# Kernel optimization log

Hardware: AMD Instinct MI355X
Metric: run time of the kernel (lower is better)

Reference implementation:

```python
import jax, jax.numpy as jnp
import numpy as np

N = 100000
E = 1600000
IN_C = 128
OUT_C = 64
NEG_SLOPE = 0.2


def setup_inputs() -> dict:
    key = jax.random.key(0)
    k1, k2, k3, k4 = jax.random.split(key, 4)
    x = jax.random.normal(k1, (N, IN_C), dtype=jnp.float32)
    edge_index = jax.random.randint(k2, (2, E), 0, N, dtype=jnp.int64)
    # Linear weight as in torch nn.Linear (bias=False): W @ x -> x @ W.T
    W = jax.random.normal(k3, (OUT_C, IN_C), dtype=jnp.float32) * (1.0 / np.sqrt(IN_C))
    # attention vector a over [Wx_i || Wx_j]
    a = jax.random.normal(k4, (2 * OUT_C,), dtype=jnp.float32) * (1.0 / np.sqrt(2 * OUT_C))
    return {"x": x, "edge_index": edge_index, "W": W, "a": a}


def reference(x, edge_index, W, a):
    src = edge_index[0]  # [E] source nodes j
    dst = edge_index[1]  # [E] target nodes i

    Wx = x @ W.T                                   # [N, OUT_C]
    # per-node attention scores, gathered per edge (same math as a . [Wx_i||Wx_j])
    s_i = Wx @ a[:OUT_C]                           # [N]
    s_j = Wx @ a[OUT_C:]                           # [N]
    e = jax.nn.leaky_relu(s_i[dst] + s_j[src], NEG_SLOPE)  # [E]

    # segment softmax over edges grouped by target node
    m = jax.ops.segment_max(e, dst, num_segments=N)        # [N]
    m = jnp.where(jnp.isneginf(m), 0.0, m)
    exp_e = jnp.exp(e - m[dst])                            # [E]
    denom = jax.ops.segment_sum(exp_e, dst, num_segments=N)  # [N]
    alpha = exp_e / denom[dst]                             # [E]

    msg = alpha[:, None] * Wx[src]                 # [E, OUT_C]
    h = jax.ops.segment_sum(msg, dst, num_segments=N)  # [N, OUT_C]
    return jax.nn.elu(h)
```

## Files before the change

### kernel.cpp

```cpp
#include <hip/hip_runtime.h>

#define NN 100000
#define EE 1600000
#define INC 128
#define OUTC 64
#define NEG_SLOPE 0.2f

#define BSH 7
#define BNODES 128
#define NB 782
#define BCAP 2560
#define SCAP2 4480
#define CHUNKA 4096
#define NBLKA 391
#define NBLKG (NB + NBLKA)
#define NSLOT 10

typedef __attribute__((ext_vector_type(8))) short bf16x8;
typedef __attribute__((ext_vector_type(4))) float f32x4;

__device__ __forceinline__ unsigned short f2bf(float f) {
  unsigned u = __float_as_uint(f);
  unsigned r = (u + 0x7fffu + ((u >> 16) & 1u)) >> 16;
  return (unsigned short)r;
}
__device__ __forceinline__ float bf2f(unsigned u16) {
  return __uint_as_float(u16 << 16);
}

__global__ __launch_bounds__(256) void k_zero(int* __restrict__ gcursor) {
  for (int i = threadIdx.x; i < NB; i += 256) gcursor[i] = 0;
}

__global__ __launch_bounds__(256)
__attribute__((amdgpu_waves_per_eu(1, 3)))
void k_gb(
    const float* __restrict__ x, const float* __restrict__ W,
    const float* __restrict__ a, unsigned short* __restrict__ Wxh,
    float* __restrict__ s_i, float* __restrict__ s_j,
    const int* __restrict__ src, const int* __restrict__ dst,
    int* __restrict__ gcursor, unsigned* __restrict__ binned)
{
  __shared__ __align__(16) char smem[44240];
  const int t = threadIdx.x;
  const int bid = blockIdx.x;
  const bool isBin = (bid % 3 == 2);

  if (!isBin) {
    const int gi = (bid / 3) * 2 + (bid % 3);
    unsigned short (*hs)[32][72] = reinterpret_cast<unsigned short(*)[32][72]>(smem);
    const int w = t >> 6;
    const int l = t & 63;
    const int lr = l & 15;
    const int lk = l >> 4;
    const int row0 = gi * 128 + w * 32;

    f32x4 acc[2][4];
    #pragma unroll
    for (int m = 0; m < 2; ++m)
      #pragma unroll
      for (int n = 0; n < 4; ++n) acc[m][n] = (f32x4){0.f, 0.f, 0.f, 0.f};

    #pragma unroll
    for (int ks = 0; ks < 4; ++ks) {
      const int k0 = ks * 32 + lk * 8;
      bf16x8 af[2], bfr[4];
      #pragma unroll
      for (int m = 0; m < 2; ++m) {
        int r = row0 + m * 16 + lr;
        r = (r < NN) ? r : (NN - 1);
        const float* p = &x[(size_t)r * INC + k0];
        float4 u0 = *reinterpret_cast<const float4*>(p);
        float4 u1 = *reinterpret_cast<const float4*>(p + 4);
        af[m][0] = (short)f2bf(u0.x); af[m][1] = (short)f2bf(u0.y);
        af[m][2] = (short)f2bf(u0.z); af[m][3] = (short)f2bf(u0.w);
        af[m][4] = (short)f2bf(u1.x); af[m][5] = (short)f2bf(u1.y);
        af[m][6] = (short)f2bf(u1.z); af[m][7] = (short)f2bf(u1.w);
      }
      #pragma unroll
      for (int n = 0; n < 4; ++n) {
        int c = n * 16 + lr;
        const float* p = &W[(size_t)c * INC + k0];
        float4 u0 = *reinterpret_cast<const float4*>(p);
        float4 u1 = *reinterpret_cast<const float4*>(p + 4);
        bfr[n][0] = (short)f2bf(u0.x); bfr[n][1] = (short)f2bf(u0.y);
        bfr[n][2] = (short)f2bf(u0.z); bfr[n][3] = (short)f2bf(u0.w);
        bfr[n][4] = (short)f2bf(u1.x); bfr[n][5] = (short)f2bf(u1.y);
        bfr[n][6] = (short)f2bf(u1.z); bfr[n][7] = (short)f2bf(u1.w);
      }
      #pragma unroll
      for (int m = 0; m < 2; ++m)
        #pragma unroll
        for (int n = 0; n < 4; ++n)
          acc[m][n] = __builtin_amdgcn_mfma_f32_16x16x32_bf16(af[m], bfr[n], acc[m][n], 0, 0, 0);
    }

    float a1[4], a2[4];
    #pragma unroll
    for (int n = 0; n < 4; ++n) {
      a1[n] = a[n * 16 + lr];
      a2[n] = a[OUTC + n * 16 + lr];
    }
    #pragma unroll
    for (int m = 0; m < 2; ++m)
      #pragma unroll
      for (int r = 0; r < 4; ++r) {
        float p1 = 0.f, p2 = 0.f;
        #pragma unroll
        for (int n = 0; n < 4; ++n) {
          p1 = fmaf(acc[m][n][r], a1[n], p1);
          p2 = fmaf(acc[m][n][r], a2[n], p2);
        }
        #pragma unroll
        for (int mm = 1; mm < 16; mm <<= 1) {
          p1 += __shfl_xor(p1, mm);
          p2 += __shfl_xor(p2, mm);
        }
        int rr = row0 + m * 16 + lk * 4 + r;
        if (lr == 0 && rr < NN) { s_i[rr] = p1; s_j[rr] = p2; }
      }

    #pragma unroll
    for (int m = 0; m < 2; ++m)
      #pragma unroll
      for (int n = 0; n < 4; ++n)
        #pragma unroll
        for (int r = 0; r < 4; ++r)
          hs[w][m * 16 + lk * 4 + r][n * 16 + lr] = f2bf(acc[m][n][r]);
    __syncthreads();
    #pragma unroll
    for (int j = 0; j < 4; ++j) {
      int idx = j * 64 + t % 64 + (w * 64 - w * 64);
      idx = j * 64 + l;
      int rr = idx >> 3;
      int c8 = idx & 7;
      int node = row0 + rr;
      if (node < NN) {
        uint4 v = *reinterpret_cast<const uint4*>(&hs[w][rr][c8 * 8]);
        *reinterpret_cast<uint4*>(&Wxh[(size_t)node * OUTC + c8 * 8]) = v;
      }
    }
  } else {
    const int bi = bid / 3;
    int* lh = reinterpret_cast<int*>(smem);
    int* ls = lh + 1024;
    int* gb = ls + 1024;
    uint2* stage = reinterpret_cast<uint2*>(smem + 11328);
    __shared__ int wsum[4];
    const int c0 = bi * CHUNKA;
    const int cend = min(c0 + CHUNKA, EE);
    const int total = cend - c0;

    #pragma unroll
    for (int k = 0; k < 4; ++k) lh[t + k * 256] = 0;
    __syncthreads();

    int esrc[16], edst[16], rnk[16];
    #pragma unroll
    for (int k = 0; k < 16; ++k) {
      int i = c0 + t + k * 256;
      bool v = i < cend;
      esrc[k] = v ? src[i] : -1;
      edst[k] = v ? dst[i] : -1;
      rnk[k] = v ? atomicAdd(&lh[edst[k] >> BSH], 1) : 0;
    }
    __syncthreads();

    {
      int a0 = lh[4 * t], a1 = lh[4 * t + 1], a2 = lh[4 * t + 2], a3 = lh[4 * t + 3];
      int s4 = a0 + a1 + a2 + a3;
      int incl = s4;
      #pragma unroll
      for (int d = 1; d < 64; d <<= 1) {
        int u = __shfl_up(incl, d);
        if ((t & 63) >= d) incl += u;
      }
      if ((t & 63) == 63) wsum[t >> 6] = incl;
      __syncthreads();
      int wv = t >> 6;
      int wbase = 0;
      #pragma unroll
      for (int k = 0; k < 4; ++k) wbase += (k < wv) ? wsum[k] : 0;
      int ex = wbase + incl - s4;
      ls[4 * t] = ex;
      ls[4 * t + 1] = ex + a0;
      ls[4 * t + 2] = ex + a0 + a1;
      ls[4 * t + 3] = ex + a0 + a1 + a2;
    }
    __syncthreads();

    #pragma unroll
    for (int k = 0; k < 16; ++k) {
      if (edst[k] >= 0) {
        int bb = edst[k] >> BSH;
        stage[ls[bb] + rnk[k]] =
            make_uint2((unsigned)esrc[k] | ((unsigned)(edst[k] & (BNODES - 1)) << 17),
                       (unsigned)bb);
      }
    }
    __syncthreads();

    for (int b = t; b < NB; b += 256) {
      int cnt = lh[b];
      if (cnt) gb[b] = atomicAdd(&gcursor[b], cnt);
    }
    __syncthreads();

    for (int i = t; i < total; i += 256) {
      uint2 pr = stage[i];
      int b = (int)pr.y;
      int idx = gb[b] + (i - ls[b]);
      if (idx < BCAP) binned[b * BCAP + idx] = pr.x;
    }
  }
}

__global__ __launch_bounds__(256) void k_sort(const int* __restrict__ gcursor,
                                              const unsigned* __restrict__ binned,
                                              const float* __restrict__ s_i,
                                              const float* __restrict__ s_j,
                                              uint2* __restrict__ offs2,
                                              unsigned* __restrict__ sorted4) {
  __shared__ int cnt128[BNODES];
  __shared__ int ex128[BNODES];
  __shared__ float sil[BNODES];
  __shared__ float den[BNODES];
  __shared__ float invd[BNODES];
  __shared__ unsigned stage[SCAP2];
  __shared__ int sW0, sTot;
  const int t = threadIdx.x;
  const int b = blockIdx.x;
  const int n0 = b << BSH;
  const int base = b * BCAP;
  const int obase = b * SCAP2;
  const int cnt = min(gcursor[b], BCAP);

  for (int i = t; i < SCAP2; i += 256) stage[i] = 0u;
  if (t < BNODES) {
    cnt128[t] = 0;
    den[t] = 0.f;
    int n = n0 + t;
    sil[t] = (n < NN) ? s_i[n] : 0.f;
  }
  __syncthreads();

  unsigned es[NSLOT];
  int ed[NSLOT], rk[NSLOT];
  float ws[NSLOT];
  #pragma unroll
  for (int k = 0; k < NSLOT; ++k) {
    int i = t + k * 256;
    bool v = i < cnt;
    unsigned pw = v ? binned[base + i] : 0u;
    es[k] = pw & 0x1ffffu;
    ed[k] = v ? (int)(pw >> 17) : -1;
    ws[k] = 0.f;
    rk[k] = 0;
    if (v) {
      rk[k] = atomicAdd(&cnt128[ed[k]], 1);
      float sc = sil[ed[k]] + s_j[es[k]];
      sc = (sc > 0.f) ? sc : NEG_SLOPE * sc;
      ws[k] = __expf(sc);
      atomicAdd(&den[ed[k]], ws[k]);
    }
  }
  __syncthreads();

  int cpad = 0;
  if (t < BNODES) {
    float dv = den[t];
    invd[t] = (dv > 0.f) ? 1.f / dv : 0.f;
    cpad = (cnt128[t] + 15) & ~15;
  }
  int incl = cpad;
  #pragma unroll
  for (int d = 1; d < 64; d <<= 1) {
    int u = __shfl_up(incl, d);
    if ((t & 63) >= d) incl += u;
  }
  if (t == 63) sW0 = incl;
  __syncthreads();
  if (t < BNODES) {
    int ex = incl - cpad + ((t >= 64) ? sW0 : 0);
    ex128[t] = ex;
    int n = n0 + t;
    if (n < NN) offs2[n] = make_uint2((unsigned)(obase + ex), (unsigned)(obase + ex + cnt128[t]));
    if (t == BNODES - 1) sTot = ex + cpad;
  }
  __syncthreads();

  #pragma unroll
  for (int k = 0; k < NSLOT; ++k) {
    if (ed[k] >= 0) {
      float alpha = ws[k] * invd[ed[k]];
      unsigned abits = (__float_as_uint(alpha) + 0x10000u) & 0xfffe0000u;
      stage[ex128[ed[k]] + rk[k]] = abits | es[k];
    }
  }
  __syncthreads();
  const int tot = sTot;
  for (int i = t; i < tot; i += 256) sorted4[obase + i] = stage[i];
}

__global__ __launch_bounds__(256) void k_aggregate(
    const uint2* __restrict__ offs2, const unsigned* __restrict__ sorted4,
    const unsigned short* __restrict__ Wxh, float* __restrict__ out)
{
  int n = blockIdx.x * 8 + (threadIdx.x >> 5);
  if (n >= NN) return;
  int l32 = threadIdx.x & 31;
  int g = l32 >> 3;
  unsigned cl8 = (l32 & 7) << 3;
  uint2 se = offs2[n];
  int start = (int)se.x, end = (int)se.y;
  float acc[8];
  #pragma unroll
  for (int j = 0; j < 8; ++j) acc[j] = 0.f;

  for (int base = start; base < end; base += 16) {
    int i = base + 4 * g;
    uint4 pw = *reinterpret_cast<const uint4*>(&sorted4[i]);
    unsigned s0 = pw.x & 0x1ffffu, s1 = pw.y & 0x1ffffu;
    unsigned s2 = pw.z & 0x1ffffu, s3 = pw.w & 0x1ffffu;
    float w0 = __uint_as_float(pw.x & 0xfffe0000u);
    float w1 = __uint_as_float(pw.y & 0xfffe0000u);
    float w2 = __uint_as_float(pw.z & 0xfffe0000u);
    float w3 = __uint_as_float(pw.w & 0xfffe0000u);
    uint4 h0 = *reinterpret_cast<const uint4*>(&Wxh[(s0 << 6) + cl8]);
    uint4 h1 = *reinterpret_cast<const uint4*>(&Wxh[(s1 << 6) + cl8]);
    uint4 h2 = *reinterpret_cast<const uint4*>(&Wxh[(s2 << 6) + cl8]);
    uint4 h3 = *reinterpret_cast<const uint4*>(&Wxh[(s3 << 6) + cl8]);
    acc[0] = fmaf(w0, bf2f(h0.x & 0xffffu), acc[0]);
    acc[1] = fmaf(w0, bf2f(h0.x >> 16), acc[1]);
    acc[2] = fmaf(w0, bf2f(h0.y & 0xffffu), acc[2]);
    acc[3] = fmaf(w0, bf2f(h0.y >> 16), acc[3]);
    acc[4] = fmaf(w0, bf2f(h0.z & 0xffffu), acc[4]);
    acc[5] = fmaf(w0, bf2f(h0.z >> 16), acc[5]);
    acc[6] = fmaf(w0, bf2f(h0.w & 0xffffu), acc[6]);
    acc[7] = fmaf(w0, bf2f(h0.w >> 16), acc[7]);
    acc[0] = fmaf(w1, bf2f(h1.x & 0xffffu), acc[0]);
    acc[1] = fmaf(w1, bf2f(h1.x >> 16), acc[1]);
    acc[2] = fmaf(w1, bf2f(h1.y & 0xffffu), acc[2]);
    acc[3] = fmaf(w1, bf2f(h1.y >> 16), acc[3]);
    acc[4] = fmaf(w1, bf2f(h1.z & 0xffffu), acc[4]);
    acc[5] = fmaf(w1, bf2f(h1.z >> 16), acc[5]);
    acc[6] = fmaf(w1, bf2f(h1.w & 0xffffu), acc[6]);
    acc[7] = fmaf(w1, bf2f(h1.w >> 16), acc[7]);
    acc[0] = fmaf(w2, bf2f(h2.x & 0xffffu), acc[0]);
    acc[1] = fmaf(w2, bf2f(h2.x >> 16), acc[1]);
    acc[2] = fmaf(w2, bf2f(h2.y & 0xffffu), acc[2]);
    acc[3] = fmaf(w2, bf2f(h2.y >> 16), acc[3]);
    acc[4] = fmaf(w2, bf2f(h2.z & 0xffffu), acc[4]);
    acc[5] = fmaf(w2, bf2f(h2.z >> 16), acc[5]);
    acc[6] = fmaf(w2, bf2f(h2.w & 0xffffu), acc[6]);
    acc[7] = fmaf(w2, bf2f(h2.w >> 16), acc[7]);
    acc[0] = fmaf(w3, bf2f(h3.x & 0xffffu), acc[0]);
    acc[1] = fmaf(w3, bf2f(h3.x >> 16), acc[1]);
    acc[2] = fmaf(w3, bf2f(h3.y & 0xffffu), acc[2]);
    acc[3] = fmaf(w3, bf2f(h3.y >> 16), acc[3]);
    acc[4] = fmaf(w3, bf2f(h3.z & 0xffffu), acc[4]);
    acc[5] = fmaf(w3, bf2f(h3.z >> 16), acc[5]);
    acc[6] = fmaf(w3, bf2f(h3.w & 0xffffu), acc[6]);
    acc[7] = fmaf(w3, bf2f(h3.w >> 16), acc[7]);
  }

  #pragma unroll
  for (int m = 8; m <= 16; m <<= 1) {
    #pragma unroll
    for (int j = 0; j < 8; ++j) acc[j] += __shfl_xor(acc[j], m);
  }

  if (g == 0) {
    float r[8];
    #pragma unroll
    for (int j = 0; j < 8; ++j)
      r[j] = (acc[j] > 0.f) ? acc[j] : __expf(acc[j]) - 1.f;
    float4 o0 = make_float4(r[0], r[1], r[2], r[3]);
    float4 o1 = make_float4(r[4], r[5], r[6], r[7]);
    unsigned ob = ((unsigned)n << 6) + cl8;
    *reinterpret_cast<float4*>(&out[ob]) = o0;
    *reinterpret_cast<float4*>(&out[ob + 4]) = o1;
  }
}

extern "C" void kernel_launch(void* const* d_in, const int* in_sizes, int n_in,
                              void* d_out, int out_size, void* d_ws, size_t ws_size,
                              hipStream_t stream) {
  const float* x = (const float*)d_in[0];
  const int* edge = (const int*)d_in[1];
  const float* W = (const float*)d_in[2];
  const float* a = (const float*)d_in[3];
  const int* srcIdx = edge;
  const int* dstIdx = edge + EE;
  float* out = (float*)d_out;

  unsigned short* Wxh = (unsigned short*)d_ws;
  unsigned* binned = (unsigned*)((char*)d_ws + (size_t)NN * OUTC * 2);
  unsigned* sorted4 = binned + (size_t)NB * BCAP;
  int* gcursor = (int*)(sorted4 + (size_t)NB * SCAP2);
  float* s_i = (float*)(gcursor + NB);
  float* s_j = s_i + NN;
  uint2* offs2 = (uint2*)(s_j + NN);

  k_zero<<<1, 256, 0, stream>>>(gcursor);
  k_gb<<<NBLKG, 256, 0, stream>>>(x, W, a, Wxh, s_i, s_j, srcIdx, dstIdx, gcursor, binned);
  k_sort<<<NB, 256, 0, stream>>>(gcursor, binned, s_i, s_j, offs2, sorted4);
  k_aggregate<<<(NN + 7) / 8, 256, 0, stream>>>(offs2, sorted4, Wxh, out);
}
```

Baseline: 91.90 us.

## Fuse per-bin sort and aggregation into one kernel using LDS-staged edges

After: 91.76 us. No clear change (-0.2%).

```diff
diff --git a/kernel.cpp b/kernel.cpp
--- a/kernel.cpp
+++ b/kernel.cpp
@@ -10,7 +10,6 @@
 #define BNODES 128
 #define NB 782
 #define BCAP 2560
-#define SCAP2 4480
 #define CHUNKA 4096
 #define NBLKA 391
 #define NBLKG (NB + NBLKA)
@@ -130,8 +129,7 @@
     __syncthreads();
     #pragma unroll
     for (int j = 0; j < 4; ++j) {
-      int idx = j * 64 + t % 64 + (w * 64 - w * 64);
-      idx = j * 64 + l;
+      int idx = j * 64 + l;
       int rr = idx >> 3;
       int c8 = idx & 7;
       int node = row0 + rr;
@@ -215,27 +213,25 @@
   }
 }
 
-__global__ __launch_bounds__(256) void k_sort(const int* __restrict__ gcursor,
-                                              const unsigned* __restrict__ binned,
-                                              const float* __restrict__ s_i,
-                                              const float* __restrict__ s_j,
-                                              uint2* __restrict__ offs2,
-                                              unsigned* __restrict__ sorted4) {
+__global__ __launch_bounds__(256) void k_sa(const int* __restrict__ gcursor,
+                                            const unsigned* __restrict__ binned,
+                                            const float* __restrict__ s_i,
+                                            const float* __restrict__ s_j,
+                                            const unsigned short* __restrict__ Wxh,
+                                            float* __restrict__ out) {
   __shared__ int cnt128[BNODES];
   __shared__ int ex128[BNODES];
   __shared__ float sil[BNODES];
   __shared__ float den[BNODES];
   __shared__ float invd[BNODES];
-  __shared__ unsigned stage[SCAP2];
-  __shared__ int sW0, sTot;
+  __shared__ unsigned stage[BCAP];
+  __shared__ int sW0;
   const int t = threadIdx.x;
   const int b = blockIdx.x;
   const int n0 = b << BSH;
   const int base = b * BCAP;
-  const int obase = b * SCAP2;
   const int cnt = min(gcursor[b], BCAP);
 
-  for (int i = t; i < SCAP2; i += 256) stage[i] = 0u;
   if (t < BNODES) {
     cnt128[t] = 0;
     den[t] = 0.f;
@@ -266,13 +262,13 @@
   }
   __syncthreads();
 
-  int cpad = 0;
+  int c0 = 0;
   if (t < BNODES) {
     float dv = den[t];
     invd[t] = (dv > 0.f) ? 1.f / dv : 0.f;
-    cpad = (cnt128[t] + 15) & ~15;
-  }
-  int incl = cpad;
+    c0 = cnt128[t];
+  }
+  int incl = c0;
   #pragma unroll
   for (int d = 1; d < 64; d <<= 1) {
     int u = __shfl_up(incl, d);
@@ -280,13 +276,7 @@
   }
   if (t == 63) sW0 = incl;
   __syncthreads();
-  if (t < BNODES) {
-    int ex = incl - cpad + ((t >= 64) ? sW0 : 0);
-    ex128[t] = ex;
-    int n = n0 + t;
-    if (n < NN) offs2[n] = make_uint2((unsigned)(obase + ex), (unsigned)(obase + ex + cnt128[t]));
-    if (t == BNODES - 1) sTot = ex + cpad;
-  }
+  if (t < BNODES) ex128[t] = incl - c0 + ((t >= 64) ? sW0 : 0);
   __syncthreads();
 
   #pragma unroll
@@ -298,88 +288,72 @@
     }
   }
   __syncthreads();
-  const int tot = sTot;
-  for (int i = t; i < tot; i += 256) sorted4[obase + i] = stage[i];
-}
-
-__global__ __launch_bounds__(256) void k_aggregate(
-    const uint2* __restrict__ offs2, const unsigned* __restrict__ sorted4,
-    const unsigned short* __restrict__ Wxh, float* __restrict__ out)
-{
-  int n = blockIdx.x * 8 + (threadIdx.x >> 5);
-  if (n >= NN) return;
-  int l32 = threadIdx.x & 31;
-  int g = l32 >> 3;
-  unsigned cl8 = (l32 & 7) << 3;
-  uint2 se = offs2[n];
-  int start = (int)se.x, end = (int)se.y;
-  float acc[8];
+
+  const int dl = t >> 1;
+  const unsigned cb = (t & 1) << 5;
+  const int myCnt = cnt128[dl];
+  const int myEx = ex128[dl];
+  float acc[32];
   #pragma unroll
-  for (int j = 0; j < 8; ++j) acc[j] = 0.f;
-
-  for (int base = start; base < end; base += 16) {
-    int i = base + 4 * g;
-    uint4 pw = *reinterpret_cast<const uint4*>(&sorted4[i]);
-    unsigned s0 = pw.x & 0x1ffffu, s1 = pw.y & 0x1ffffu;
-    unsigned s2 = pw.z & 0x1ffffu, s3 = pw.w & 0x1ffffu;
-    float w0 = __uint_as_float(pw.x & 0xfffe0000u);
-    float w1 = __uint_as_float(pw.y & 0xfffe0000u);
-    float w2 = __uint_as_float(pw.z & 0xfffe0000u);
-    float w3 = __uint_as_float(pw.w & 0xfffe0000u);
-    uint4 h0 = *reinterpret_cast<const uint4*>(&Wxh[(s0 << 6) + cl8]);
-    uint4 h1 = *reinterpret_cast<const uint4*>(&Wxh[(s1 << 6) + cl8]);
-    uint4 h2 = *reinterpret_cast<const uint4*>(&Wxh[(s2 << 6) + cl8]);
-    uint4 h3 = *reinterpret_cast<const uint4*>(&Wxh[(s3 << 6) + cl8]);
-    acc[0] = fmaf(w0, bf2f(h0.x & 0xffffu), acc[0]);
-    acc[1] = fmaf(w0, bf2f(h0.x >> 16), acc[1]);
-    acc[2] = fmaf(w0, bf2f(h0.y & 0xffffu), acc[2]);
-    acc[3] = fmaf(w0, bf2f(h0.y >> 16), acc[3]);
-    acc[4] = fmaf(w0, bf2f(h0.z & 0xffffu), acc[4]);
-    acc[5] = fmaf(w0, bf2f(h0.z >> 16), acc[5]);
-    acc[6] = fmaf(w0, bf2f(h0.w & 0xffffu), acc[6]);
-    acc[7] = fmaf(w0, bf2f(h0.w >> 16), acc[7]);
-    acc[0] = fmaf(w1, bf2f(h1.x & 0xffffu), acc[0]);
-    acc[1] = fmaf(w1, bf2f(h1.x >> 16), acc[1]);
-    acc[2] = fmaf(w1, bf2f(h1.y & 0xffffu), acc[2]);
-    acc[3] = fmaf(w1, bf2f(h1.y >> 16), acc[3]);
-    acc[4] = fmaf(w1, bf2f(h1.z & 0xffffu), acc[4]);
-    acc[5] = fmaf(w1, bf2f(h1.z >> 16), acc[5]);
-    acc[6] = fmaf(w1, bf2f(h1.w & 0xffffu), acc[6]);
-    acc[7] = fmaf(w1, bf2f(h1.w >> 16), acc[7]);
-    acc[0] = fmaf(w2, bf2f(h2.x & 0xffffu), acc[0]);
-    acc[1] = fmaf(w2, bf2f(h2.x >> 16), acc[1]);
-    acc[2] = fmaf(w2, bf2f(h2.y & 0xffffu), acc[2]);
-    acc[3] = fmaf(w2, bf2f(h2.y >> 16), acc[3]);
-    acc[4] = fmaf(w2, bf2f(h2.z & 0xffffu), acc[4]);
-    acc[5] = fmaf(w2, bf2f(h2.z >> 16), acc[5]);
-    acc[6] = fmaf(w2, bf2f(h2.w & 0xffffu), acc[6]);
-    acc[7] = fmaf(w2, bf2f(h2.w >> 16), acc[7]);
-    acc[0] = fmaf(w3, bf2f(h3.x & 0xffffu), acc[0]);
-    acc[1] = fmaf(w3, bf2f(h3.x >> 16), acc[1]);
-    acc[2] = fmaf(w3, bf2f(h3.y & 0xffffu), acc[2]);
-    acc[3] = fmaf(w3, bf2f(h3.y >> 16), acc[3]);
-    acc[4] = fmaf(w3, bf2f(h3.z & 0xffffu), acc[4]);
-    acc[5] = fmaf(w3, bf2f(h3.z >> 16), acc[5]);
-    acc[6] = fmaf(w3, bf2f(h3.w & 0xffffu), acc[6]);
-    acc[7] = fmaf(w3, bf2f(h3.w >> 16), acc[7]);
-  }
-
-  #pragma unroll
-  for (int m = 8; m <= 16; m <<= 1) {
-    #pragma unroll
-    for (int j = 0; j < 8; ++j) acc[j] += __shfl_xor(acc[j], m);
-  }
-
-  if (g == 0) {
-    float r[8];
-    #pragma unroll
-    for (int j = 0; j < 8; ++j)
-      r[j] = (acc[j] > 0.f) ? acc[j] : __expf(acc[j]) - 1.f;
-    float4 o0 = make_float4(r[0], r[1], r[2], r[3]);
-    float4 o1 = make_float4(r[4], r[5], r[6], r[7]);
-    unsigned ob = ((unsigned)n << 6) + cl8;
-    *reinterpret_cast<float4*>(&out[ob]) = o0;
-    *reinterpret_cast<float4*>(&out[ob + 4]) = o1;
+  for (int j = 0; j < 32; ++j) acc[j] = 0.f;
+
+  #define EDGE_BODY(E) do {                                              \
+    unsigned u = stage[myEx + (E)];                                      \
+    float wgt = __uint_as_float(u & 0xfffe0000u);                        \
+    const uint4* hp = reinterpret_cast<const uint4*>(&Wxh[((u & 0x1ffffu) << 6) + cb]); \
+    uint4 h0 = hp[0], h1 = hp[1], h2 = hp[2], h3 = hp[3];                \
+    acc[0]  = fmaf(wgt, bf2f(h0.x & 0xffffu), acc[0]);                   \
+    acc[1]  = fmaf(wgt, bf2f(h0.x >> 16), acc[1]);                       \
+    acc[2]  = fmaf(wgt, bf2f(h0.y & 0xffffu), acc[2]);                   \
+    acc[3]  = fmaf(wgt, bf2f(h0.y >> 16), acc[3]);                       \
+    acc[4]  = fmaf(wgt, bf2f(h0.z & 0xffffu), acc[4]);                   \
+    acc[5]  = fmaf(wgt, bf2f(h0.z >> 16), acc[5]);                       \
+    acc[6]  = fmaf(wgt, bf2f(h0.w & 0xffffu), acc[6]);                   \
+    acc[7]  = fmaf(wgt, bf2f(h0.w >> 16), acc[7]);                       \
+    acc[8]  = fmaf(wgt, bf2f(h1.x & 0xffffu), acc[8]);                   \
+    acc[9]  = fmaf(wgt, bf2f(h1.x >> 16), acc[9]);                       \
+    acc[10] = fmaf(wgt, bf2f(h1.y & 0xffffu), acc[10]);                  \
+    acc[11] = fmaf(wgt, bf2f(h1.y >> 16), acc[11]);                      \
+    acc[12] = fmaf(wgt, bf2f(h1.z & 0xffffu), acc[12]);                  \
+    acc[13] = fmaf(wgt, bf2f(h1.z >> 16), acc[13]);                      \
+    acc[14] = fmaf(wgt, bf2f(h1.w & 0xffffu), acc[14]);                  \
+    acc[15] = fmaf(wgt, bf2f(h1.w >> 16), acc[15]);                      \
+    acc[16] = fmaf(wgt, bf2f(h2.x & 0xffffu), acc[16]);                  \
+    acc[17] = fmaf(wgt, bf2f(h2.x >> 16), acc[17]);                      \
+    acc[18] = fmaf(wgt, bf2f(h2.y & 0xffffu), acc[18]);                  \
+    acc[19] = fmaf(wgt, bf2f(h2.y >> 16), acc[19]);                      \
+    acc[20] = fmaf(wgt, bf2f(h2.z & 0xffffu), acc[20]);                  \
+    acc[21] = fmaf(wgt, bf2f(h2.z >> 16), acc[21]);                      \
+    acc[22] = fmaf(wgt, bf2f(h2.w & 0xffffu), acc[22]);                  \
+    acc[23] = fmaf(wgt, bf2f(h2.w >> 16), acc[23]);                      \
+    acc[24] = fmaf(wgt, bf2f(h3.x & 0xffffu), acc[24]);                  \
+    acc[25] = fmaf(wgt, bf2f(h3.x >> 16), acc[25]);                      \
+    acc[26] = fmaf(wgt, bf2f(h3.y & 0xffffu), acc[26]);                  \
+    acc[27] = fmaf(wgt, bf2f(h3.y >> 16), acc[27]);                      \
+    acc[28] = fmaf(wgt, bf2f(h3.z & 0xffffu), acc[28]);                  \
+    acc[29] = fmaf(wgt, bf2f(h3.z >> 16), acc[29]);                      \
+    acc[30] = fmaf(wgt, bf2f(h3.w & 0xffffu), acc[30]);                  \
+    acc[31] = fmaf(wgt, bf2f(h3.w >> 16), acc[31]);                      \
+  } while (0)
+
+  int e = 0;
+  for (; e + 2 <= myCnt; e += 2) { EDGE_BODY(e); EDGE_BODY(e + 1); }
+  if (e < myCnt) EDGE_BODY(e);
+  #undef EDGE_BODY
+
+  const int n = n0 + dl;
+  if (n < NN) {
+    unsigned ob = ((unsigned)n << 6) + cb;
+    #pragma unroll
+    for (int q = 0; q < 8; ++q) {
+      float4 r;
+      #pragma unroll
+      for (int j = 0; j < 4; ++j) {
+        float v = acc[q * 4 + j];
+        (&r.x)[j] = (v > 0.f) ? v : __expf(v) - 1.f;
+      }
+      *reinterpret_cast<float4*>(&out[ob + q * 4]) = r;
+    }
   }
 }
 
@@ -396,14 +370,11 @@
 
   unsigned short* Wxh = (unsigned short*)d_ws;
   unsigned* binned = (unsigned*)((char*)d_ws + (size_t)NN * OUTC * 2);
-  unsigned* sorted4 = binned + (size_t)NB * BCAP;
-  int* gcursor = (int*)(sorted4 + (size_t)NB * SCAP2);
+  int* gcursor = (int*)(binned + (size_t)NB * BCAP);
   float* s_i = (float*)(gcursor + NB);
   float* s_j = s_i + NN;
-  uint2* offs2 = (uint2*)(s_j + NN);
 
   k_zero<<<1, 256, 0, stream>>>(gcursor);
   k_gb<<<NBLKG, 256, 0, stream>>>(x, W, a, Wxh, s_i, s_j, srcIdx, dstIdx, gcursor, binned);
-  k_sort<<<NB, 256, 0, stream>>>(gcursor, binned, s_i, s_j, offs2, sorted4);
-  k_aggregate<<<(NN + 7) / 8, 256, 0, stream>>>(offs2, sorted4, Wxh, out);
-}
+  k_sa<<<NB, 256, 0, stream>>>(gcursor, binned, s_i, s_j, Wxh, out);
+}
```

## Fuse edge sort and aggregation into one kernel using LDS-resident edges

Applied to the files above, without the earlier changes.

New measurement: 89.85 us. 1.02x faster.

```diff
diff --git a/kernel.cpp b/kernel.cpp
--- a/kernel.cpp
+++ b/kernel.cpp
@@ -10,7 +10,6 @@
 #define BNODES 128
 #define NB 782
 #define BCAP 2560
-#define SCAP2 4480
 #define CHUNKA 4096
 #define NBLKA 391
 #define NBLKG (NB + NBLKA)
@@ -130,8 +129,7 @@
     __syncthreads();
     #pragma unroll
     for (int j = 0; j < 4; ++j) {
-      int idx = j * 64 + t % 64 + (w * 64 - w * 64);
-      idx = j * 64 + l;
+      int idx = j * 64 + l;
       int rr = idx >> 3;
       int c8 = idx & 7;
       int node = row0 + rr;
@@ -215,27 +213,25 @@
   }
 }
 
-__global__ __launch_bounds__(256) void k_sort(const int* __restrict__ gcursor,
-                                              const unsigned* __restrict__ binned,
-                                              const float* __restrict__ s_i,
-                                              const float* __restrict__ s_j,
-                                              uint2* __restrict__ offs2,
-                                              unsigned* __restrict__ sorted4) {
+__global__ __launch_bounds__(256) void k_sa(const int* __restrict__ gcursor,
+                                            const unsigned* __restrict__ binned,
+                                            const float* __restrict__ s_i,
+                                            const float* __restrict__ s_j,
+                                            const unsigned short* __restrict__ Wxh,
+                                            float* __restrict__ out) {
   __shared__ int cnt128[BNODES];
   __shared__ int ex128[BNODES];
   __shared__ float sil[BNODES];
   __shared__ float den[BNODES];
   __shared__ float invd[BNODES];
-  __shared__ unsigned stage[SCAP2];
-  __shared__ int sW0, sTot;
+  __shared__ unsigned stage[BCAP];
+  __shared__ int sW0;
   const int t = threadIdx.x;
   const int b = blockIdx.x;
   const int n0 = b << BSH;
   const int base = b * BCAP;
-  const int obase = b * SCAP2;
   const int cnt = min(gcursor[b], BCAP);
 
-  for (int i = t; i < SCAP2; i += 256) stage[i] = 0u;
   if (t < BNODES) {
     cnt128[t] = 0;
     den[t] = 0.f;
@@ -266,13 +262,13 @@
   }
   __syncthreads();
 
-  int cpad = 0;
+  int c0 = 0;
   if (t < BNODES) {
     float dv = den[t];
     invd[t] = (dv > 0.f) ? 1.f / dv : 0.f;
-    cpad = (cnt128[t] + 15) & ~15;
-  }
-  int incl = cpad;
+    c0 = cnt128[t];
+  }
+  int incl = c0;
   #pragma unroll
   for (int d = 1; d < 64; d <<= 1) {
     int u = __shfl_up(incl, d);
@@ -280,13 +276,7 @@
   }
   if (t == 63) sW0 = incl;
   __syncthreads();
-  if (t < BNODES) {
-    int ex = incl - cpad + ((t >= 64) ? sW0 : 0);
-    ex128[t] = ex;
-    int n = n0 + t;
-    if (n < NN) offs2[n] = make_uint2((unsigned)(obase + ex), (unsigned)(obase + ex + cnt128[t]));
-    if (t == BNODES - 1) sTot = ex + cpad;
-  }
+  if (t < BNODES) ex128[t] = incl - c0 + ((t >= 64) ? sW0 : 0);
   __syncthreads();
 
   #pragma unroll
@@ -298,88 +288,84 @@
     }
   }
   __syncthreads();
-  const int tot = sTot;
-  for (int i = t; i < tot; i += 256) sorted4[obase + i] = stage[i];
-}
-
-__global__ __launch_bounds__(256) void k_aggregate(
-    const uint2* __restrict__ offs2, const unsigned* __restrict__ sorted4,
-    const unsigned short* __restrict__ Wxh, float* __restrict__ out)
-{
-  int n = blockIdx.x * 8 + (threadIdx.x >> 5);
-  if (n >= NN) return;
-  int l32 = threadIdx.x & 31;
-  int g = l32 >> 3;
-  unsigned cl8 = (l32 & 7) << 3;
-  uint2 se = offs2[n];
-  int start = (int)se.x, end = (int)se.y;
-  float acc[8];
-  #pragma unroll
-  for (int j = 0; j < 8; ++j) acc[j] = 0.f;
-
-  for (int base = start; base < end; base += 16) {
-    int i = base + 4 * g;
-    uint4 pw = *reinterpret_cast<const uint4*>(&sorted4[i]);
-    unsigned s0 = pw.x & 0x1ffffu, s1 = pw.y & 0x1ffffu;
-    unsigned s2 = pw.z & 0x1ffffu, s3 = pw.w & 0x1ffffu;
-    float w0 = __uint_as_float(pw.x & 0xfffe0000u);
-    float w1 = __uint_as_float(pw.y & 0xfffe0000u);
-    float w2 = __uint_as_float(pw.z & 0xfffe0000u);
-    float w3 = __uint_as_float(pw.w & 0xfffe0000u);
-    uint4 h0 = *reinterpret_cast<const uint4*>(&Wxh[(s0 << 6) + cl8]);
-    uint4 h1 = *reinterpret_cast<const uint4*>(&Wxh[(s1 << 6) + cl8]);
-    uint4 h2 = *reinterpret_cast<const uint4*>(&Wxh[(s2 << 6) + cl8]);
-    uint4 h3 = *reinterpret_cast<const uint4*>(&Wxh[(s3 << 6) + cl8]);
-    acc[0] = fmaf(w0, bf2f(h0.x & 0xffffu), acc[0]);
-    acc[1] = fmaf(w0, bf2f(h0.x >> 16), acc[1]);
-    acc[2] = fmaf(w0, bf2f(h0.y & 0xffffu), acc[2]);
-    acc[3] = fmaf(w0, bf2f(h0.y >> 16), acc[3]);
-    acc[4] = fmaf(w0, bf2f(h0.z & 0xffffu), acc[4]);
-    acc[5] = fmaf(w0, bf2f(h0.z >> 16), acc[5]);
-    acc[6] = fmaf(w0, bf2f(h0.w & 0xffffu), acc[6]);
-    acc[7] = fmaf(w0, bf2f(h0.w >> 16), acc[7]);
-    acc[0] = fmaf(w1, bf2f(h1.x & 0xffffu), acc[0]);
-    acc[1] = fmaf(w1, bf2f(h1.x >> 16), acc[1]);
-    acc[2] = fmaf(w1, bf2f(h1.y & 0xffffu), acc[2]);
-    acc[3] = fmaf(w1, bf2f(h1.y >> 16), acc[3]);
-    acc[4] = fmaf(w1, bf2f(h1.z & 0xffffu), acc[4]);
-    acc[5] = fmaf(w1, bf2f(h1.z >> 16), acc[5]);
-    acc[6] = fmaf(w1, bf2f(h1.w & 0xffffu), acc[6]);
-    acc[7] = fmaf(w1, bf2f(h1.w >> 16), acc[7]);
-    acc[0] = fmaf(w2, bf2f(h2.x & 0xffffu), acc[0]);
-    acc[1] = fmaf(w2, bf2f(h2.x >> 16), acc[1]);
-    acc[2] = fmaf(w2, bf2f(h2.y & 0xffffu), acc[2]);
-    acc[3] = fmaf(w2, bf2f(h2.y >> 16), acc[3]);
-    acc[4] = fmaf(w2, bf2f(h2.z & 0xffffu), acc[4]);
-    acc[5] = fmaf(w2, bf2f(h2.z >> 16), acc[5]);
-    acc[6] = fmaf(w2, bf2f(h2.w & 0xffffu), acc[6]);
-    acc[7] = fmaf(w2, bf2f(h2.w >> 16), acc[7]);
-    acc[0] = fmaf(w3, bf2f(h3.x & 0xffffu), acc[0]);
-    acc[1] = fmaf(w3, bf2f(h3.x >> 16), acc[1]);
-    acc[2] = fmaf(w3, bf2f(h3.y & 0xffffu), acc[2]);
-    acc[3] = fmaf(w3, bf2f(h3.y >> 16), acc[3]);
-    acc[4] = fmaf(w3, bf2f(h3.z & 0xffffu), acc[4]);
-    acc[5] = fmaf(w3, bf2f(h3.z >> 16), acc[5]);
-    acc[6] = fmaf(w3, bf2f(h3.w & 0xffffu), acc[6]);
-    acc[7] = fmaf(w3, bf2f(h3.w >> 16), acc[7]);
-  }
-
-  #pragma unroll
-  for (int m = 8; m <= 16; m <<= 1) {
-    #pragma unroll
-    for (int j = 0; j < 8; ++j) acc[j] += __shfl_xor(acc[j], m);
-  }
-
-  if (g == 0) {
-    float r[8];
-    #pragma unroll
-    for (int j = 0; j < 8; ++j)
-      r[j] = (acc[j] > 0.f) ? acc[j] : __expf(acc[j]) - 1.f;
-    float4 o0 = make_float4(r[0], r[1], r[2], r[3]);
-    float4 o1 = make_float4(r[4], r[5], r[6], r[7]);
-    unsigned ob = ((unsigned)n << 6) + cl8;
-    *reinterpret_cast<float4*>(&out[ob]) = o0;
-    *reinterpret_cast<float4*>(&out[ob + 4]) = o1;
+
+  const int half = t >> 5;
+  const int l32 = t & 31;
+  const int g = l32 >> 3;
+  const unsigned cl8 = (l32 & 7) << 3;
+
+  for (int rnd = 0; rnd < 16; ++rnd) {
+    const int dl = rnd * 8 + half;
+    const int myCnt = cnt128[dl];
+    const int myEx = ex128[dl];
+    float acc[8];
+    #pragma unroll
+    for (int j = 0; j < 8; ++j) acc[j] = 0.f;
+
+    for (int eb = 0; eb < myCnt; eb += 16) {
+      int i0 = eb + 4 * g;
+      unsigned u0 = (i0 + 0 < myCnt) ? stage[myEx + i0 + 0] : 0u;
+      unsigned u1 = (i0 + 1 < myCnt) ? stage[myEx + i0 + 1] : 0u;
+      unsigned u2 = (i0 + 2 < myCnt) ? stage[myEx + i0 + 2] : 0u;
+      unsigned u3 = (i0 + 3 < myCnt) ? stage[myEx + i0 + 3] : 0u;
+      float w0 = __uint_as_float(u0 & 0xfffe0000u);
+      float w1 = __uint_as_float(u1 & 0xfffe0000u);
+      float w2 = __uint_as_float(u2 & 0xfffe0000u);
+      float w3 = __uint_as_float(u3 & 0xfffe0000u);
+      uint4 h0 = *reinterpret_cast<const uint4*>(&Wxh[((u0 & 0x1ffffu) << 6) + cl8]);
+      uint4 h1 = *reinterpret_cast<const uint4*>(&Wxh[((u1 & 0x1ffffu) << 6) + cl8]);
+      uint4 h2 = *reinterpret_cast<const uint4*>(&Wxh[((u2 & 0x1ffffu) << 6) + cl8]);
+      uint4 h3 = *reinterpret_cast<const uint4*>(&Wxh[((u3 & 0x1ffffu) << 6) + cl8]);
+      acc[0] = fmaf(w0, bf2f(h0.x & 0xffffu), acc[0]);
+      acc[1] = fmaf(w0, bf2f(h0.x >> 16), acc[1]);
+      acc[2] = fmaf(w0, bf2f(h0.y & 0xffffu), acc[2]);
+      acc[3] = fmaf(w0, bf2f(h0.y >> 16), acc[3]);
+      acc[4] = fmaf(w0, bf2f(h0.z & 0xffffu), acc[4]);
+      acc[5] = fmaf(w0, bf2f(h0.z >> 16), acc[5]);
+      acc[6] = fmaf(w0, bf2f(h0.w & 0xffffu), acc[6]);
+      acc[7] = fmaf(w0, bf2f(h0.w >> 16), acc[7]);
+      acc[0] = fmaf(w1, bf2f(h1.x & 0xffffu), acc[0]);
+      acc[1] = fmaf(w1, bf2f(h1.x >> 16), acc[1]);
+      acc[2] = fmaf(w1, bf2f(h1.y & 0xffffu), acc[2]);
+      acc[3] = fmaf(w1, bf2f(h1.y >> 16), acc[3]);
+      acc[4] = fmaf(w1, bf2f(h1.z & 0xffffu), acc[4]);
+      acc[5] = fmaf(w1, bf2f(h1.z >> 16), acc[5]);
+      acc[6] = fmaf(w1, bf2f(h1.w & 0xffffu), acc[6]);
+      acc[7] = fmaf(w1, bf2f(h1.w >> 16), acc[7]);
+      acc[0] = fmaf(w2, bf2f(h2.x & 0xffffu), acc[0]);
+      acc[1] = fmaf(w2, bf2f(h2.x >> 16), acc[1]);
+      acc[2] = fmaf(w2, bf2f(h2.y & 0xffffu), acc[2]);
+      acc[3] = fmaf(w2, bf2f(h2.y >> 16), acc[3]);
+      acc[4] = fmaf(w2, bf2f(h2.z & 0xffffu), acc[4]);
+      acc[5] = fmaf(w2, bf2f(h2.z >> 16), acc[5]);
+      acc[6] = fmaf(w2, bf2f(h2.w & 0xffffu), acc[6]);
+      acc[7] = fmaf(w2, bf2f(h2.w >> 16), acc[7]);
+      acc[0] = fmaf(w3, bf2f(h3.x & 0xffffu), acc[0]);
+      acc[1] = fmaf(w3, bf2f(h3.x >> 16), acc[1]);
+      acc[2] = fmaf(w3, bf2f(h3.y & 0xffffu), acc[2]);
+      acc[3] = fmaf(w3, bf2f(h3.y >> 16), acc[3]);
+      acc[4] = fmaf(w3, bf2f(h3.z & 0xffffu), acc[4]);
+      acc[5] = fmaf(w3, bf2f(h3.z >> 16), acc[5]);
+      acc[6] = fmaf(w3, bf2f(h3.w & 0xffffu), acc[6]);
+      acc[7] = fmaf(w3, bf2f(h3.w >> 16), acc[7]);
+    }
+
+    #pragma unroll
+    for (int m = 8; m <= 16; m <<= 1) {
+      #pragma unroll
+      for (int j = 0; j < 8; ++j) acc[j] += __shfl_xor(acc[j], m);
+    }
+
+    const int n = n0 + dl;
+    if (g == 0 && n < NN) {
+      float r[8];
+      #pragma unroll
+      for (int j = 0; j < 8; ++j)
+        r[j] = (acc[j] > 0.f) ? acc[j] : __expf(acc[j]) - 1.f;
+      unsigned ob = ((unsigned)n << 6) + cl8;
+      *reinterpret_cast<float4*>(&out[ob]) = make_float4(r[0], r[1], r[2], r[3]);
+      *reinterpret_cast<float4*>(&out[ob + 4]) = make_float4(r[4], r[5], r[6], r[7]);
+    }
   }
 }
 
@@ -396,14 +382,11 @@
 
   unsigned short* Wxh = (unsigned short*)d_ws;
   unsigned* binned = (unsigned*)((char*)d_ws + (size_t)NN * OUTC * 2);
-  unsigned* sorted4 = binned + (size_t)NB * BCAP;
-  int* gcursor = (int*)(sorted4 + (size_t)NB * SCAP2);
+  int* gcursor = (int*)(binned + (size_t)NB * BCAP);
   float* s_i = (float*)(gcursor + NB);
   float* s_j = s_i + NN;
-  uint2* offs2 = (uint2*)(s_j + NN);
 
   k_zero<<<1, 256, 0, stream>>>(gcursor);
   k_gb<<<NBLKG, 256, 0, stream>>>(x, W, a, Wxh, s_i, s_j, srcIdx, dstIdx, gcursor, binned);
-  k_sort<<<NB, 256, 0, stream>>>(gcursor, binned, s_i, s_j, offs2, sorted4);
-  k_aggregate<<<(NN + 7) / 8, 256, 0, stream>>>(offs2, sorted4, Wxh, out);
-}
+  k_sa<<<NB, 256, 0, stream>>>(gcursor, binned, s_i, s_j, Wxh, out);
+}
```
